# Optimization experiments

Hardware: AMD Instinct MI355X
Metric: run time of the kernel (lower is better)

The kernel has to match this reference:

```python
import jax, jax.numpy as jnp
import numpy as np

B, P, N, C = 8192, 64, 32, 10

def setup_inputs() -> dict:
    key = jax.random.key(0)
    k1, k2 = jax.random.split(key)
    x = jax.random.normal(k1, (B, P, N), dtype=jnp.float32)
    weight = jax.random.normal(k2, (C, P * N), dtype=jnp.float32)
    return {"x": x, "weight": weight}

def reference(x, weight):
    # x: [B, P, N] -> [B, P*N]; weight: [C, P*N]
    xf = x.reshape(x.shape[0], -1)
    w = jax.nn.log_softmax(weight, axis=1)          # [C, D]
    # logsumexp over D of x[b,d] + w[c,d] -> [B, C]
    return jax.nn.logsumexp(xf[:, None, :] + w[None, :, :], axis=2)
```

## Files before the change

kernel.cpp:

```cpp
#include <hip/hip_runtime.h>

constexpr int B = 8192;
constexpr int D = 2048;
constexpr int C = 10;
constexpr int D4 = D / 4;

__global__ __launch_bounds__(256) void softmax_w_kernel(
    const float* __restrict__ w, float* __restrict__ p) {
  const int c = blockIdx.x;
  const int t = threadIdx.x;
  const int lane = t & 63, wid = t >> 6;

  const float4* wr = reinterpret_cast<const float4*>(w + c * D);
  float4 v0 = wr[t];
  float4 v1 = wr[t + 256];

  float m = fmaxf(fmaxf(fmaxf(v0.x, v0.y), fmaxf(v0.z, v0.w)),
                  fmaxf(fmaxf(v1.x, v1.y), fmaxf(v1.z, v1.w)));
#pragma unroll
  for (int o = 1; o < 64; o <<= 1) m = fmaxf(m, __shfl_xor(m, o));
  __shared__ float sred[4];
  if (lane == 0) sred[wid] = m;
  __syncthreads();
  m = fmaxf(fmaxf(sred[0], sred[1]), fmaxf(sred[2], sred[3]));
  __syncthreads();

  float4 e0, e1;
  e0.x = __expf(v0.x - m); e0.y = __expf(v0.y - m);
  e0.z = __expf(v0.z - m); e0.w = __expf(v0.w - m);
  e1.x = __expf(v1.x - m); e1.y = __expf(v1.y - m);
  e1.z = __expf(v1.z - m); e1.w = __expf(v1.w - m);

  float s = (e0.x + e0.y + e0.z + e0.w) + (e1.x + e1.y + e1.z + e1.w);
#pragma unroll
  for (int o = 1; o < 64; o <<= 1) s += __shfl_xor(s, o);
  if (lane == 0) sred[wid] = s;
  __syncthreads();
  s = (sred[0] + sred[1]) + (sred[2] + sred[3]);

  const float inv = 1.0f / s;
  float4 q0 = {e0.x * inv, e0.y * inv, e0.z * inv, e0.w * inv};
  float4 q1 = {e1.x * inv, e1.y * inv, e1.z * inv, e1.w * inv};
  float4* pr = reinterpret_cast<float4*>(p + c * D);
  pr[t] = q0;
  pr[t + 256] = q1;
}

__global__ __launch_bounds__(512, 2) void lse_main_kernel(
    const float* __restrict__ x, const float* __restrict__ p,
    float* __restrict__ out) {
  __shared__ float4 plds[C * D4];

  const int t = threadIdx.x;
  const int lane = t & 63, wid = t >> 6;

#pragma unroll
  for (int k = 0; k < C * D4 / 512; ++k)
    plds[k * 512 + t] = reinterpret_cast<const float4*>(p)[k * 512 + t];
  __syncthreads();

  const int row0 = blockIdx.x * 16 + wid * 2;
  const float4* xr = reinterpret_cast<const float4*>(x + (size_t)row0 * D);

  float acc0[C], acc1[C];
#pragma unroll
  for (int c = 0; c < C; ++c) { acc0[c] = 0.0f; acc1[c] = 0.0f; }

  float4 nx0 = xr[lane];
  float4 nx1 = xr[D4 + lane];

#pragma unroll 1
  for (int j = 0; j < 8; ++j) {
    const float4 cx0 = nx0, cx1 = nx1;
    const int fn = ((j + 1) & 7) * 64 + lane;
    nx0 = xr[fn];
    nx1 = xr[D4 + fn];

    float4 e0, e1;
    e0.x = __expf(cx0.x); e0.y = __expf(cx0.y);
    e0.z = __expf(cx0.z); e0.w = __expf(cx0.w);
    e1.x = __expf(cx1.x); e1.y = __expf(cx1.y);
    e1.z = __expf(cx1.z); e1.w = __expf(cx1.w);

    const int f4 = j * 64 + lane;
#pragma unroll
    for (int c = 0; c < C; ++c) {
      const float4 pv = plds[c * D4 + f4];
      acc0[c] += e0.x * pv.x + e0.y * pv.y + e0.z * pv.z + e0.w * pv.w;
      acc1[c] += e1.x * pv.x + e1.y * pv.y + e1.z * pv.z + e1.w * pv.w;
    }
  }

#pragma unroll
  for (int c = 0; c < C; ++c) {
    float v0 = acc0[c], v1 = acc1[c];
#pragma unroll
    for (int o = 1; o < 64; o <<= 1) {
      v0 += __shfl_xor(v0, o);
      v1 += __shfl_xor(v1, o);
    }
    if (lane == c) {
      out[(size_t)row0 * C + c] = logf(v0);
      out[(size_t)(row0 + 1) * C + c] = logf(v1);
    }
  }
}

extern "C" void kernel_launch(void* const* d_in, const int* in_sizes, int n_in,
                              void* d_out, int out_size, void* d_ws, size_t ws_size,
                              hipStream_t stream) {
  const float* x = (const float*)d_in[0];
  const float* w = (const float*)d_in[1];
  float* out = (float*)d_out;
  float* p = (float*)d_ws;

  softmax_w_kernel<<<C, 256, 0, stream>>>(w, p);
  lse_main_kernel<<<B / 16, 512, 0, stream>>>(x, p, out);
}
```

Measured before the change: 100.8 us.

## Split feature dimension across two wave groups with LDS partial-sum reduction

Blocks grow to 1024 threads. Two groups of eight waves each process half of the 2048-wide feature dimension for the same 16 rows, so each wave runs half as many loop iterations. Partial sums go through shared memory, reusing the weight buffer after a barrier, and a final pass adds the two halves and takes the log. The goal is more resident waves per CU to hide load and exp latency. In exchange it adds two block barriers and a tighter register budget from the (1024, 8) launch bounds, which could cause spills.

```diff
diff --git a/kernel.cpp b/kernel.cpp
--- a/kernel.cpp
+++ b/kernel.cpp
@@ -4,6 +4,7 @@
 constexpr int D = 2048;
 constexpr int C = 10;
 constexpr int D4 = D / 4;
+constexpr int HD4 = D4 / 2;
 
 __global__ __launch_bounds__(256) void softmax_w_kernel(
     const float* __restrict__ w, float* __restrict__ p) {
@@ -46,33 +47,36 @@
   pr[t + 256] = q1;
 }
 
-__global__ __launch_bounds__(512, 2) void lse_main_kernel(
+__global__ __launch_bounds__(1024, 8) void lse_main_kernel(
     const float* __restrict__ x, const float* __restrict__ p,
     float* __restrict__ out) {
   __shared__ float4 plds[C * D4];
 
   const int t = threadIdx.x;
-  const int lane = t & 63, wid = t >> 6;
+  const int lane = t & 63, w = t >> 6;
 
 #pragma unroll
-  for (int k = 0; k < C * D4 / 512; ++k)
-    plds[k * 512 + t] = reinterpret_cast<const float4*>(p)[k * 512 + t];
+  for (int k = 0; k < 5; ++k)
+    plds[k * 1024 + t] = reinterpret_cast<const float4*>(p)[k * 1024 + t];
   __syncthreads();
 
-  const int row0 = blockIdx.x * 16 + wid * 2;
+  const int h = w >> 3;
+  const int rp = w & 7;
+  const int row0 = blockIdx.x * 16 + rp * 2;
+  const int base = h * HD4;
   const float4* xr = reinterpret_cast<const float4*>(x + (size_t)row0 * D);
 
   float acc0[C], acc1[C];
 #pragma unroll
   for (int c = 0; c < C; ++c) { acc0[c] = 0.0f; acc1[c] = 0.0f; }
 
-  float4 nx0 = xr[lane];
-  float4 nx1 = xr[D4 + lane];
+  float4 nx0 = xr[base + lane];
+  float4 nx1 = xr[D4 + base + lane];
 
 #pragma unroll 1
-  for (int j = 0; j < 8; ++j) {
+  for (int j = 0; j < 4; ++j) {
     const float4 cx0 = nx0, cx1 = nx1;
-    const int fn = ((j + 1) & 7) * 64 + lane;
+    const int fn = base + ((j + 1) & 3) * 64 + lane;
     nx0 = xr[fn];
     nx1 = xr[D4 + fn];
 
@@ -82,14 +86,18 @@
     e1.x = __expf(cx1.x); e1.y = __expf(cx1.y);
     e1.z = __expf(cx1.z); e1.w = __expf(cx1.w);
 
-    const int f4 = j * 64 + lane;
+    const int f4i = base + j * 64 + lane;
 #pragma unroll
     for (int c = 0; c < C; ++c) {
-      const float4 pv = plds[c * D4 + f4];
+      const float4 pv = plds[c * D4 + f4i];
       acc0[c] += e0.x * pv.x + e0.y * pv.y + e0.z * pv.z + e0.w * pv.w;
       acc1[c] += e1.x * pv.x + e1.y * pv.y + e1.z * pv.z + e1.w * pv.w;
     }
   }
+
+  __syncthreads();
+
+  float* part = reinterpret_cast<float*>(plds);
 
 #pragma unroll
   for (int c = 0; c < C; ++c) {
@@ -100,9 +108,16 @@
       v1 += __shfl_xor(v1, o);
     }
     if (lane == c) {
-      out[(size_t)row0 * C + c] = logf(v0);
-      out[(size_t)(row0 + 1) * C + c] = logf(v1);
+      part[((rp * 2 + 0) * C + c) * 2 + h] = v0;
+      part[((rp * 2 + 1) * C + c) * 2 + h] = v1;
     }
+  }
+  __syncthreads();
+
+  if (t < 16 * C) {
+    const int row = t / C, c = t % C;
+    const float s = part[(row * C + c) * 2] + part[(row * C + c) * 2 + 1];
+    out[(size_t)(blockIdx.x * 16 + row) * C + c] = logf(s);
   }
 }
 
@@ -115,5 +130,5 @@
   float* p = (float*)d_ws;
 
   softmax_w_kernel<<<C, 256, 0, stream>>>(w, p);
-  lse_main_kernel<<<B / 16, 512, 0, stream>>>(x, p, out);
+  lse_main_kernel<<<B / 16, 1024, 0, stream>>>(x, p, out);
 }
```

Result: slower. 107.8 us (+7.0%).
